# Optimization experiments

Measured on AMD Instinct MI355X. Metric: run time of the kernel, lower is better.

## Reference

```python
import jax, jax.numpy as jnp
import numpy as np

B, N, D, H = 4, 512, 256, 256


def setup_inputs() -> dict:
    key = jax.random.key(0)
    ks = jax.random.split(key, 8)
    s = lambda fan: 1.0 / np.sqrt(fan)
    return {
        "X": jax.random.normal(ks[0], (B, N, D), dtype=jnp.float32),
        "Y": jax.random.normal(ks[1], (B, N, D), dtype=jnp.float32),
        # fc = Linear(D,H) -> Tanh -> Linear(H,H)
        "W1": jax.random.normal(ks[2], (H, D), dtype=jnp.float32) * s(D),
        "b1": jnp.zeros((H,), dtype=jnp.float32),
        "W2": jax.random.normal(ks[3], (H, H), dtype=jnp.float32) * s(H),
        "b2": jnp.zeros((H,), dtype=jnp.float32),
        # fc_q, fc_k
        "Wq": jax.random.normal(ks[4], (H, H), dtype=jnp.float32) * s(H),
        "bq": jnp.zeros((H,), dtype=jnp.float32),
        "Wk": jax.random.normal(ks[5], (H, H), dtype=jnp.float32) * s(H),
        "bk": jnp.zeros((H,), dtype=jnp.float32),
        # AddComp projection vector v: E_ij = v . tanh(Q_i + K_j)
        "v": jax.random.normal(ks[6], (H,), dtype=jnp.float32) * s(H),
        "k": 5,
    }


def reference(X, Y, W1, b1, W2, b2, Wq, bq, Wk, bk, v, k):
    # fc: Linear -> Tanh -> Linear  (Y and k are unused, as in the original)
    h = jnp.tanh(jnp.einsum('bnd,hd->bnh', X, W1) + b1)
    h = jnp.einsum('bnh,gh->bng', h, W2) + b2          # [B,N,H]
    Q = jnp.einsum('bnh,gh->bng', h, Wq) + bq          # [B,N,H]
    K = jnp.einsum('bnh,gh->bng', h, Wk) + bk          # [B,N,H]
    # Additive compatibility: E[b,i,j] = v . tanh(Q[b,i] + K[b,j])
    E = jnp.einsum('bijh,h->bij', jnp.tanh(Q[:, :, None, :] + K[:, None, :, :]), v)
    # Symmetrize
    return 0.5 * (E + jnp.swapaxes(E, -2, -1))
```

## Files before the change

kernel.cpp:

```cpp
#include <hip/hip_runtime.h>


typedef float f2 __attribute__((ext_vector_type(2)));
typedef float f4 __attribute__((ext_vector_type(4)));
typedef float f32x4 __attribute__((ext_vector_type(4)));
typedef __bf16 bf16x8 __attribute__((ext_vector_type(8)));

#define C2F 2.8853900817779268f

__device__ inline unsigned short f2bf(float f) {
    unsigned u = __float_as_uint(f);
    unsigned r = (u + 0x7fffu + ((u >> 16) & 1u)) >> 16;
    return (unsigned short)r;
}
__device__ inline float bf2f(unsigned short h) {
    return __uint_as_float(((unsigned)h) << 16);
}

__device__ inline void split4(const f4 a, unsigned short* hp, unsigned short* lp) {
    unsigned short h[4], l[4];
#pragma unroll
    for (int t = 0; t < 4; ++t) {
        h[t] = f2bf(a[t]);
        l[t] = f2bf(a[t] - bf2f(h[t]));
    }
    uint2 hv, lv;
    hv.x = (unsigned)h[0] | ((unsigned)h[1] << 16);
    hv.y = (unsigned)h[2] | ((unsigned)h[3] << 16);
    lv.x = (unsigned)l[0] | ((unsigned)l[1] << 16);
    lv.y = (unsigned)l[2] | ((unsigned)l[3] << 16);
    *(uint2*)hp = hv;
    *(uint2*)lp = lv;
}

template <int ACT>
__global__ __launch_bounds__(256) void gemm_fullk(
    const float* __restrict__ A, const float* __restrict__ Wa,
    const float* __restrict__ Wb, const float* __restrict__ ba,
    const float* __restrict__ bb2, float* __restrict__ C, int Nn) {
    __shared__ unsigned short sAhi[64][264];
    __shared__ unsigned short sAlo[64][264];
    __shared__ unsigned short sBhi[64][264];
    __shared__ unsigned short sBlo[64][264];

    const int tid = threadIdx.x;
    const int m0 = blockIdx.x << 6;
    const int n0 = blockIdx.y << 6;

    const float* Atile = A + (size_t)m0 * 256;
    const float* Wtile = (n0 < 256) ? (Wa + (size_t)n0 * 256)
                                    : (Wb + (size_t)(n0 - 256) * 256);
    const int col4 = (tid & 63) << 2;
    const int rgrp = tid >> 6;
#pragma unroll
    for (int t = 0; t < 16; ++t) {
        const int row = (t << 2) + rgrp;
        f4 av = *(const f4*)&Atile[(size_t)row * 256 + col4];
        f4 wv = *(const f4*)&Wtile[(size_t)row * 256 + col4];
        split4(av, &sAhi[row][col4], &sAlo[row][col4]);
        split4(wv, &sBhi[row][col4], &sBlo[row][col4]);
    }
    __syncthreads();

    const int lane = tid & 63;
    const int wav = tid >> 6;
    const int wm = wav >> 1, wn = wav & 1;
    const int fr = lane & 15;
    const int fks = (lane >> 4) << 3;

    f32x4 acc[2][2];
#pragma unroll
    for (int i = 0; i < 2; ++i)
#pragma unroll
        for (int j = 0; j < 2; ++j) acc[i][j] = (f32x4){0.f, 0.f, 0.f, 0.f};

#pragma unroll
    for (int kt = 0; kt < 256; kt += 32) {
        bf16x8 ah[2], al[2], bh[2], bl[2];
#pragma unroll
        for (int s = 0; s < 2; ++s) {
            ah[s] = *(const bf16x8*)&sAhi[(wm << 5) + (s << 4) + fr][kt + fks];
            al[s] = *(const bf16x8*)&sAlo[(wm << 5) + (s << 4) + fr][kt + fks];
            bh[s] = *(const bf16x8*)&sBhi[(wn << 5) + (s << 4) + fr][kt + fks];
            bl[s] = *(const bf16x8*)&sBlo[(wn << 5) + (s << 4) + fr][kt + fks];
        }
#pragma unroll
        for (int i = 0; i < 2; ++i)
#pragma unroll
            for (int j = 0; j < 2; ++j) {
                acc[i][j] = __builtin_amdgcn_mfma_f32_16x16x32_bf16(ah[i], bh[j], acc[i][j], 0, 0, 0);
                acc[i][j] = __builtin_amdgcn_mfma_f32_16x16x32_bf16(ah[i], bl[j], acc[i][j], 0, 0, 0);
                acc[i][j] = __builtin_amdgcn_mfma_f32_16x16x32_bf16(al[i], bh[j], acc[i][j], 0, 0, 0);
            }
    }

    const int rbase = (lane >> 4) << 2;
#pragma unroll
    for (int i = 0; i < 2; ++i) {
#pragma unroll
        for (int j = 0; j < 2; ++j) {
            const int gcol = n0 + (wn << 5) + (j << 4) + fr;
            const float bias = (ACT == 2 && gcol >= 256) ? bb2[gcol - 256] : ba[gcol];
#pragma unroll
            for (int q = 0; q < 4; ++q) {
                const int grow = m0 + (wm << 5) + (i << 4) + rbase + q;
                float x = acc[i][j][q] + bias;
                if (ACT == 1)
                    x = 1.0f - 2.0f * __builtin_amdgcn_rcpf(
                                          1.0f + __builtin_amdgcn_exp2f(C2F * x));
                if (ACT == 2) x = __builtin_amdgcn_exp2f(C2F * x);
                C[(size_t)grow * Nn + gcol] = x;
            }
        }
    }
}

__global__ __launch_bounds__(256) void gemm_nt_fullk(
    const float* __restrict__ Wq, const float* __restrict__ Wk,
    const float* __restrict__ W2, const float* __restrict__ b2,
    const float* __restrict__ bq, const float* __restrict__ bk,
    float* __restrict__ Wc, float* __restrict__ bc) {
    __shared__ unsigned short sAhi[64][264];
    __shared__ unsigned short sAlo[64][264];
    __shared__ unsigned short sBhi[64][264];
    __shared__ unsigned short sBlo[64][264];
    __shared__ float sred[64][4];

    const int tid = threadIdx.x;
    const int m0 = blockIdx.x << 6;
    const int n0 = blockIdx.y << 6;

    const float* Atile = (m0 < 256) ? (Wq + (size_t)m0 * 256)
                                    : (Wk + (size_t)(m0 - 256) * 256);
    const int col4 = (tid & 63) << 2;
    const int rgrp = tid >> 6;
#pragma unroll
    for (int t = 0; t < 16; ++t) {
        const int row = (t << 2) + rgrp;
        f4 av = *(const f4*)&Atile[(size_t)row * 256 + col4];
        split4(av, &sAhi[row][col4], &sAlo[row][col4]);
    }
    const int c4 = (tid & 15) << 2;
    const int kg = tid >> 4;
#pragma unroll
    for (int t = 0; t < 16; ++t) {
        const int k = (t << 4) + kg;
        f4 wv = *(const f4*)&W2[(size_t)k * 256 + n0 + c4];
#pragma unroll
        for (int q = 0; q < 4; ++q) {
            unsigned short hi = f2bf(wv[q]);
            sBhi[c4 + q][k] = hi;
            sBlo[c4 + q][k] = f2bf(wv[q] - bf2f(hi));
        }
    }
    __syncthreads();

    const int lane = tid & 63;
    const int wav = tid >> 6;
    const int wm = wav >> 1, wn = wav & 1;
    const int fr = lane & 15;
    const int fks = (lane >> 4) << 3;

    f32x4 acc[2][2];
#pragma unroll
    for (int i = 0; i < 2; ++i)
#pragma unroll
        for (int j = 0; j < 2; ++j) acc[i][j] = (f32x4){0.f, 0.f, 0.f, 0.f};

#pragma unroll
    for (int kt = 0; kt < 256; kt += 32) {
        bf16x8 ah[2], al[2], bh[2], bl[2];
#pragma unroll
        for (int s = 0; s < 2; ++s) {
            ah[s] = *(const bf16x8*)&sAhi[(wm << 5) + (s << 4) + fr][kt + fks];
            al[s] = *(const bf16x8*)&sAlo[(wm << 5) + (s << 4) + fr][kt + fks];
            bh[s] = *(const bf16x8*)&sBhi[(wn << 5) + (s << 4) + fr][kt + fks];
            bl[s] = *(const bf16x8*)&sBlo[(wn << 5) + (s << 4) + fr][kt + fks];
        }
#pragma unroll
        for (int i = 0; i < 2; ++i)
#pragma unroll
            for (int j = 0; j < 2; ++j) {
                acc[i][j] = __builtin_amdgcn_mfma_f32_16x16x32_bf16(ah[i], bh[j], acc[i][j], 0, 0, 0);
                acc[i][j] = __builtin_amdgcn_mfma_f32_16x16x32_bf16(ah[i], bl[j], acc[i][j], 0, 0, 0);
                acc[i][j] = __builtin_amdgcn_mfma_f32_16x16x32_bf16(al[i], bh[j], acc[i][j], 0, 0, 0);
            }
    }

    const int rbase = (lane >> 4) << 2;
#pragma unroll
    for (int i = 0; i < 2; ++i)
#pragma unroll
        for (int j = 0; j < 2; ++j) {
            const int gcol = n0 + (wn << 5) + (j << 4) + fr;
#pragma unroll
            for (int q = 0; q < 4; ++q) {
                const int grow = m0 + (wm << 5) + (i << 4) + rbase + q;
                Wc[(size_t)grow * 256 + gcol] = acc[i][j][q];
            }
        }

    if (blockIdx.y == 0) {
        const int rr = tid >> 2;
        const int part = (tid & 3) << 6;
        const int grow = m0 + rr;
        const float* Ar = (grow < 256) ? &Wq[(size_t)grow * 256]
                                       : &Wk[(size_t)(grow - 256) * 256];
        float s = 0.f;
#pragma unroll
        for (int e = 0; e < 64; e += 4) {
            f4 a = *(const f4*)&Ar[part + e];
            f4 bv = *(const f4*)&b2[part + e];
            s += a[0] * bv[0] + a[1] * bv[1] + a[2] * bv[2] + a[3] * bv[3];
        }
        sred[rr][tid & 3] = s;
        __syncthreads();
        if (tid < 64) {
            float bias = sred[tid][0] + sred[tid][1] + sred[tid][2] + sred[tid][3];
            const int g2 = m0 + tid;
            bias += (g2 < 256) ? bq[g2] : bk[g2 - 256];
            bc[g2] = bias;
        }
    }
}

__global__ __launch_bounds__(512, 4) void pairwise_kernel(
    const float* __restrict__ uwb, const float* __restrict__ v,
    float* __restrict__ out) {
    __shared__ float sU[2][64][68];
    __shared__ float sW[2][64][68];
    __shared__ float sV[128];

    const int tid = threadIdx.x;
    const int bb = blockIdx.x;
    const int hh = (bb & 1) << 7;
    const int tt = bb >> 1;
    const int b = tt >> 6;
    const int i0 = ((tt >> 3) & 7) << 6;
    const int j0 = (tt & 7) << 6;

    const float* ubase = uwb + (size_t)((b << 9) + i0) * 512 + hh;
    const float* wbase = uwb + (size_t)((b << 9) + j0) * 512 + 256 + hh;

    const int sr = tid >> 3;
    const int sc = (tid & 7) << 3;

    {
        f4 a0 = *(const f4*)&ubase[(size_t)sr * 512 + sc];
        f4 a1 = *(const f4*)&ubase[(size_t)sr * 512 + sc + 4];
        f4 b0 = *(const f4*)&wbase[(size_t)sr * 512 + sc];
        f4 b1 = *(const f4*)&wbase[(size_t)sr * 512 + sc + 4];
        *(f4*)&sU[0][sr][sc] = a0;
        *(f4*)&sU[0][sr][sc + 4] = a1;
        *(f4*)&sW[0][sr][sc] = b0;
        *(f4*)&sW[0][sr][sc + 4] = b1;
    }
    if (tid < 32) *(f4*)&sV[tid << 2] = *(const f4*)&v[hh + (tid << 2)];
    __syncthreads();

    const int ty = tid >> 5;
    const int tx = tid & 31;

    float acc[4][2];
#pragma unroll
    for (int d = 0; d < 4; ++d)
#pragma unroll
        for (int e = 0; e < 2; ++e) acc[d][e] = 0.f;

    const f2 one2 = (f2){1.f, 1.f};

#define COMPUTE_CHUNK(buf, vb)                                                  \
    {                                                                           \
        _Pragma("unroll 2") for (int h4 = 0; h4 < 64; h4 += 4) {                \
            f4 vv = *(const f4*)&sV[(vb) + h4];                                 \
            f4 uu[4], ww[2];                                                    \
            _Pragma("unroll") for (int d = 0; d < 4; ++d)                       \
                uu[d] = *(const f4*)&sU[buf][ty + (d << 4)][h4];                \
            _Pragma("unroll") for (int e = 0; e < 2; ++e)                       \
                ww[e] = *(const f4*)&sW[buf][tx + (e << 5)][h4];                \
            _Pragma("unroll") for (int d = 0; d < 4; ++d)                       \
            _Pragma("unroll") for (int e = 0; e < 2; ++e) {                     \
                f2 u01 = (f2){uu[d][0], uu[d][1]};                              \
                f2 u23 = (f2){uu[d][2], uu[d][3]};                              \
                f2 w01 = (f2){ww[e][0], ww[e][1]};                              \
                f2 w23 = (f2){ww[e][2], ww[e][3]};                              \
                f2 p1 = __builtin_elementwise_fma(u01, w01, one2);              \
                f2 p2 = __builtin_elementwise_fma(u23, w23, one2);              \
                float den1 = p1[0] * p1[1];                                     \
                float den2 = p2[0] * p2[1];                                     \
                float num1 = fmaf(vv[1], p1[0], vv[0] * p1[1]);                 \
                float num2 = fmaf(vv[3], p2[0], vv[2] * p2[1]);                 \
                acc[d][e] = fmaf(num1, __builtin_amdgcn_rcpf(den1), acc[d][e]); \
                acc[d][e] = fmaf(num2, __builtin_amdgcn_rcpf(den2), acc[d][e]); \
            }                                                                   \
        }                                                                       \
    }

    f4 pa0 = *(const f4*)&ubase[(size_t)sr * 512 + 64 + sc];
    f4 pa1 = *(const f4*)&ubase[(size_t)sr * 512 + 64 + sc + 4];
    f4 pb0 = *(const f4*)&wbase[(size_t)sr * 512 + 64 + sc];
    f4 pb1 = *(const f4*)&wbase[(size_t)sr * 512 + 64 + sc + 4];

    COMPUTE_CHUNK(0, 0)

    *(f4*)&sU[1][sr][sc] = pa0;
    *(f4*)&sU[1][sr][sc + 4] = pa1;
    *(f4*)&sW[1][sr][sc] = pb0;
    *(f4*)&sW[1][sr][sc + 4] = pb1;
    __syncthreads();

    COMPUTE_CHUNK(1, 64)
#undef COMPUTE_CHUNK

    float sv = 0.f;
#pragma unroll
    for (int k = 0; k < 128; k += 4) {
        f4 t = *(const f4*)&sV[k];
        sv += (t[0] + t[1]) + (t[2] + t[3]);
    }

    float c[4][2];
#pragma unroll
    for (int d = 0; d < 4; ++d)
#pragma unroll
        for (int e = 0; e < 2; ++e) c[d][e] = fmaf(0.5f, sv, -acc[d][e]);

    float* obase = out + (size_t)((b << 9) + i0) * 512 + j0;
#pragma unroll
    for (int d = 0; d < 4; ++d)
#pragma unroll
        for (int e = 0; e < 2; ++e)
            atomicAdd(&obase[(size_t)(ty + (d << 4)) * 512 + tx + (e << 5)], c[d][e]);

    float(*sT)[68] = sU[0];
#pragma unroll
    for (int d = 0; d < 4; ++d)
#pragma unroll
        for (int e = 0; e < 2; ++e)
            sT[ty + (d << 4)][tx + (e << 5)] = c[d][e];
    __syncthreads();

    const int wv_ = tid >> 6;
    const int lane = tid & 63;
    float* mbase = out + (size_t)((b << 9) + j0) * 512 + i0;
#pragma unroll
    for (int it = 0; it < 8; ++it) {
        const int r = (it << 3) + wv_;
        atomicAdd(&mbase[(size_t)r * 512 + lane], sT[lane][r]);
    }
}

extern "C" void kernel_launch(void* const* d_in, const int* in_sizes, int n_in,
                              void* d_out, int out_size, void* d_ws, size_t ws_size,
                              hipStream_t stream) {
    const float* X  = (const float*)d_in[0];
    const float* W1 = (const float*)d_in[2];
    const float* b1 = (const float*)d_in[3];
    const float* W2 = (const float*)d_in[4];
    const float* b2 = (const float*)d_in[5];
    const float* Wq = (const float*)d_in[6];
    const float* bq = (const float*)d_in[7];
    const float* Wk = (const float*)d_in[8];
    const float* bk = (const float*)d_in[9];
    const float* v  = (const float*)d_in[10];

    float* ws  = (float*)d_ws;
    float* h1  = ws;
    float* uwb = ws + 524288;
    float* Wc  = ws + 1572864;
    float* bc  = ws + 1703936;
    float* out = (float*)d_out;

    hipMemsetAsync(out, 0, (size_t)out_size * sizeof(float), stream);

    gemm_nt_fullk<<<dim3(8, 4), 256, 0, stream>>>(Wq, Wk, W2, b2, bq, bk, Wc, bc);
    gemm_fullk<1><<<dim3(32, 4), 256, 0, stream>>>(X, W1, W1, b1, b1, h1, 256);
    gemm_fullk<2><<<dim3(32, 8), 256, 0, stream>>>(h1, Wc, Wc + 65536, bc, bc + 256, uwb, 512);
    pairwise_kernel<<<512, 512, 0, stream>>>(uwb, v, out);
}
```

Measured before the change: 69.89 us.

## Merge first-stage GEMMs, pair rational tanh terms, replace atomics with symmetrize pass

Folds the Wc/bc weight-fusion GEMM and the X·W1 tanh GEMM into one launch, so the two independent first-stage matmuls share a single grid. The pairwise kernel now combines four h-terms per reciprocal instead of two, halving the rcp count. It also stops using memset and atomics: each half-H block writes its partial E to workspace, and a new kernel sums the halves, transposes, and symmetrizes. The exp output is clamped to 1e4 so the larger product of four factors does not overflow, at some cost in accuracy for large arguments. The new path adds a workspace round trip and an extra launch.

```diff
diff --git a/kernel.cpp b/kernel.cpp
--- a/kernel.cpp
+++ b/kernel.cpp
@@ -108,17 +108,20 @@
                 if (ACT == 1)
                     x = 1.0f - 2.0f * __builtin_amdgcn_rcpf(
                                           1.0f + __builtin_amdgcn_exp2f(C2F * x));
-                if (ACT == 2) x = __builtin_amdgcn_exp2f(C2F * x);
+                if (ACT == 2)
+                    x = fminf(__builtin_amdgcn_exp2f(C2F * x), 1.0e4f);
                 C[(size_t)grow * Nn + gcol] = x;
             }
         }
     }
 }
 
-__global__ __launch_bounds__(256) void gemm_nt_fullk(
-    const float* __restrict__ Wq, const float* __restrict__ Wk,
-    const float* __restrict__ W2, const float* __restrict__ b2,
-    const float* __restrict__ bq, const float* __restrict__ bk,
+__global__ __launch_bounds__(256) void gemm_stage1(
+    const float* __restrict__ X, const float* __restrict__ W1,
+    const float* __restrict__ b1, const float* __restrict__ Wq,
+    const float* __restrict__ Wk, const float* __restrict__ W2,
+    const float* __restrict__ b2, const float* __restrict__ bq,
+    const float* __restrict__ bk, float* __restrict__ h1,
     float* __restrict__ Wc, float* __restrict__ bc) {
     __shared__ unsigned short sAhi[64][264];
     __shared__ unsigned short sAlo[64][264];
@@ -127,30 +130,46 @@
     __shared__ float sred[64][4];
 
     const int tid = threadIdx.x;
-    const int m0 = blockIdx.x << 6;
-    const int n0 = blockIdx.y << 6;
-
-    const float* Atile = (m0 < 256) ? (Wq + (size_t)m0 * 256)
-                                    : (Wk + (size_t)(m0 - 256) * 256);
+    const bool is_nt = (blockIdx.x >= 128);
+    const int blk = is_nt ? (blockIdx.x - 128) : blockIdx.x;
+    const int m0 = (is_nt ? (blk >> 2) : (blk >> 2)) << 6;
+    const int n0 = (blk & 3) << 6;
+
     const int col4 = (tid & 63) << 2;
     const int rgrp = tid >> 6;
-#pragma unroll
-    for (int t = 0; t < 16; ++t) {
-        const int row = (t << 2) + rgrp;
-        f4 av = *(const f4*)&Atile[(size_t)row * 256 + col4];
-        split4(av, &sAhi[row][col4], &sAlo[row][col4]);
-    }
-    const int c4 = (tid & 15) << 2;
-    const int kg = tid >> 4;
-#pragma unroll
-    for (int t = 0; t < 16; ++t) {
-        const int k = (t << 4) + kg;
-        f4 wv = *(const f4*)&W2[(size_t)k * 256 + n0 + c4];
-#pragma unroll
-        for (int q = 0; q < 4; ++q) {
-            unsigned short hi = f2bf(wv[q]);
-            sBhi[c4 + q][k] = hi;
-            sBlo[c4 + q][k] = f2bf(wv[q] - bf2f(hi));
+
+    if (!is_nt) {
+        const float* Atile = X + (size_t)m0 * 256;
+        const float* Wtile = W1 + (size_t)n0 * 256;
+#pragma unroll
+        for (int t = 0; t < 16; ++t) {
+            const int row = (t << 2) + rgrp;
+            f4 av = *(const f4*)&Atile[(size_t)row * 256 + col4];
+            f4 wv = *(const f4*)&Wtile[(size_t)row * 256 + col4];
+            split4(av, &sAhi[row][col4], &sAlo[row][col4]);
+            split4(wv, &sBhi[row][col4], &sBlo[row][col4]);
+        }
+    } else {
+        const float* Atile = (m0 < 256) ? (Wq + (size_t)m0 * 256)
+                                        : (Wk + (size_t)(m0 - 256) * 256);
+#pragma unroll
+        for (int t = 0; t < 16; ++t) {
+            const int row = (t << 2) + rgrp;
+            f4 av = *(const f4*)&Atile[(size_t)row * 256 + col4];
+            split4(av, &sAhi[row][col4], &sAlo[row][col4]);
+        }
+        const int c4 = (tid & 15) << 2;
+        const int kg = tid >> 4;
+#pragma unroll
+        for (int t = 0; t < 16; ++t) {
+            const int k = (t << 4) + kg;
+            f4 wv = *(const f4*)&W2[(size_t)k * 256 + n0 + c4];
+#pragma unroll
+            for (int q = 0; q < 4; ++q) {
+                unsigned short hi = f2bf(wv[q]);
+                sBhi[c4 + q][k] = hi;
+                sBlo[c4 + q][k] = f2bf(wv[q] - bf2f(hi));
+            }
         }
     }
     __syncthreads();
@@ -188,45 +207,62 @@
     }
 
     const int rbase = (lane >> 4) << 2;
-#pragma unroll
-    for (int i = 0; i < 2; ++i)
-#pragma unroll
-        for (int j = 0; j < 2; ++j) {
-            const int gcol = n0 + (wn << 5) + (j << 4) + fr;
-#pragma unroll
-            for (int q = 0; q < 4; ++q) {
-                const int grow = m0 + (wm << 5) + (i << 4) + rbase + q;
-                Wc[(size_t)grow * 256 + gcol] = acc[i][j][q];
-            }
-        }
-
-    if (blockIdx.y == 0) {
-        const int rr = tid >> 2;
-        const int part = (tid & 3) << 6;
-        const int grow = m0 + rr;
-        const float* Ar = (grow < 256) ? &Wq[(size_t)grow * 256]
-                                       : &Wk[(size_t)(grow - 256) * 256];
-        float s = 0.f;
-#pragma unroll
-        for (int e = 0; e < 64; e += 4) {
-            f4 a = *(const f4*)&Ar[part + e];
-            f4 bv = *(const f4*)&b2[part + e];
-            s += a[0] * bv[0] + a[1] * bv[1] + a[2] * bv[2] + a[3] * bv[3];
-        }
-        sred[rr][tid & 3] = s;
-        __syncthreads();
-        if (tid < 64) {
-            float bias = sred[tid][0] + sred[tid][1] + sred[tid][2] + sred[tid][3];
-            const int g2 = m0 + tid;
-            bias += (g2 < 256) ? bq[g2] : bk[g2 - 256];
-            bc[g2] = bias;
+    if (!is_nt) {
+#pragma unroll
+        for (int i = 0; i < 2; ++i)
+#pragma unroll
+            for (int j = 0; j < 2; ++j) {
+                const int gcol = n0 + (wn << 5) + (j << 4) + fr;
+                const float bias = b1[gcol];
+#pragma unroll
+                for (int q = 0; q < 4; ++q) {
+                    const int grow = m0 + (wm << 5) + (i << 4) + rbase + q;
+                    float x = acc[i][j][q] + bias;
+                    x = 1.0f - 2.0f * __builtin_amdgcn_rcpf(
+                                          1.0f + __builtin_amdgcn_exp2f(C2F * x));
+                    h1[(size_t)grow * 256 + gcol] = x;
+                }
+            }
+    } else {
+#pragma unroll
+        for (int i = 0; i < 2; ++i)
+#pragma unroll
+            for (int j = 0; j < 2; ++j) {
+                const int gcol = n0 + (wn << 5) + (j << 4) + fr;
+#pragma unroll
+                for (int q = 0; q < 4; ++q) {
+                    const int grow = m0 + (wm << 5) + (i << 4) + rbase + q;
+                    Wc[(size_t)grow * 256 + gcol] = acc[i][j][q];
+                }
+            }
+        if ((blk & 3) == 0) {
+            const int rr = tid >> 2;
+            const int part = (tid & 3) << 6;
+            const int grow = m0 + rr;
+            const float* Ar = (grow < 256) ? &Wq[(size_t)grow * 256]
+                                           : &Wk[(size_t)(grow - 256) * 256];
+            float s = 0.f;
+#pragma unroll
+            for (int e = 0; e < 64; e += 4) {
+                f4 a = *(const f4*)&Ar[part + e];
+                f4 bv = *(const f4*)&b2[part + e];
+                s += a[0] * bv[0] + a[1] * bv[1] + a[2] * bv[2] + a[3] * bv[3];
+            }
+            sred[rr][tid & 3] = s;
+            __syncthreads();
+            if (tid < 64) {
+                float bias = sred[tid][0] + sred[tid][1] + sred[tid][2] + sred[tid][3];
+                const int g2 = m0 + tid;
+                bias += (g2 < 256) ? bq[g2] : bk[g2 - 256];
+                bc[g2] = bias;
+            }
         }
     }
 }
 
 __global__ __launch_bounds__(512, 4) void pairwise_kernel(
     const float* __restrict__ uwb, const float* __restrict__ v,
-    float* __restrict__ out) {
+    float* __restrict__ Ep) {
     __shared__ float sU[2][64][68];
     __shared__ float sW[2][64][68];
     __shared__ float sV[128];
@@ -269,31 +305,32 @@
 
     const f2 one2 = (f2){1.f, 1.f};
 
-#define COMPUTE_CHUNK(buf, vb)                                                  \
-    {                                                                           \
-        _Pragma("unroll 2") for (int h4 = 0; h4 < 64; h4 += 4) {                \
-            f4 vv = *(const f4*)&sV[(vb) + h4];                                 \
-            f4 uu[4], ww[2];                                                    \
-            _Pragma("unroll") for (int d = 0; d < 4; ++d)                       \
-                uu[d] = *(const f4*)&sU[buf][ty + (d << 4)][h4];                \
-            _Pragma("unroll") for (int e = 0; e < 2; ++e)                       \
-                ww[e] = *(const f4*)&sW[buf][tx + (e << 5)][h4];                \
-            _Pragma("unroll") for (int d = 0; d < 4; ++d)                       \
-            _Pragma("unroll") for (int e = 0; e < 2; ++e) {                     \
-                f2 u01 = (f2){uu[d][0], uu[d][1]};                              \
-                f2 u23 = (f2){uu[d][2], uu[d][3]};                              \
-                f2 w01 = (f2){ww[e][0], ww[e][1]};                              \
-                f2 w23 = (f2){ww[e][2], ww[e][3]};                              \
-                f2 p1 = __builtin_elementwise_fma(u01, w01, one2);              \
-                f2 p2 = __builtin_elementwise_fma(u23, w23, one2);              \
-                float den1 = p1[0] * p1[1];                                     \
-                float den2 = p2[0] * p2[1];                                     \
-                float num1 = fmaf(vv[1], p1[0], vv[0] * p1[1]);                 \
-                float num2 = fmaf(vv[3], p2[0], vv[2] * p2[1]);                 \
-                acc[d][e] = fmaf(num1, __builtin_amdgcn_rcpf(den1), acc[d][e]); \
-                acc[d][e] = fmaf(num2, __builtin_amdgcn_rcpf(den2), acc[d][e]); \
-            }                                                                   \
-        }                                                                       \
+#define COMPUTE_CHUNK(buf, vb)                                                 \
+    {                                                                          \
+        _Pragma("unroll 2") for (int h4 = 0; h4 < 64; h4 += 4) {               \
+            f4 vv = *(const f4*)&sV[(vb) + h4];                                \
+            f4 uu[4], ww[2];                                                   \
+            _Pragma("unroll") for (int d = 0; d < 4; ++d)                      \
+                uu[d] = *(const f4*)&sU[buf][ty + (d << 4)][h4];               \
+            _Pragma("unroll") for (int e = 0; e < 2; ++e)                      \
+                ww[e] = *(const f4*)&sW[buf][tx + (e << 5)][h4];               \
+            _Pragma("unroll") for (int d = 0; d < 4; ++d)                      \
+            _Pragma("unroll") for (int e = 0; e < 2; ++e) {                    \
+                f2 u01 = (f2){uu[d][0], uu[d][1]};                             \
+                f2 u23 = (f2){uu[d][2], uu[d][3]};                             \
+                f2 w01 = (f2){ww[e][0], ww[e][1]};                             \
+                f2 w23 = (f2){ww[e][2], ww[e][3]};                             \
+                f2 A01 = __builtin_elementwise_fma(u01, w01, one2);            \
+                f2 A23 = __builtin_elementwise_fma(u23, w23, one2);            \
+                float m01 = A01.x * A01.y;                                     \
+                float m23 = A23.x * A23.y;                                     \
+                float P = m01 * m23;                                           \
+                float t01 = fmaf(vv[0], A01.y, vv[1] * A01.x);                 \
+                float t23 = fmaf(vv[2], A23.y, vv[3] * A23.x);                 \
+                float Nm = fmaf(t01, m23, t23 * m01);                          \
+                acc[d][e] = fmaf(Nm, __builtin_amdgcn_rcpf(P), acc[d][e]);     \
+            }                                                                  \
+        }                                                                      \
     }
 
     f4 pa0 = *(const f4*)&ubase[(size_t)sr * 512 + 64 + sc];
@@ -312,41 +349,47 @@
     COMPUTE_CHUNK(1, 64)
 #undef COMPUTE_CHUNK
 
-    float sv = 0.f;
-#pragma unroll
-    for (int k = 0; k < 128; k += 4) {
-        f4 t = *(const f4*)&sV[k];
-        sv += (t[0] + t[1]) + (t[2] + t[3]);
-    }
-
-    float c[4][2];
+    float* ep = Ep + (size_t)(bb & 1) * 1048576 +
+                (size_t)((b << 9) + i0) * 512 + j0;
 #pragma unroll
     for (int d = 0; d < 4; ++d)
 #pragma unroll
-        for (int e = 0; e < 2; ++e) c[d][e] = fmaf(0.5f, sv, -acc[d][e]);
-
-    float* obase = out + (size_t)((b << 9) + i0) * 512 + j0;
-#pragma unroll
-    for (int d = 0; d < 4; ++d)
-#pragma unroll
         for (int e = 0; e < 2; ++e)
-            atomicAdd(&obase[(size_t)(ty + (d << 4)) * 512 + tx + (e << 5)], c[d][e]);
-
-    float(*sT)[68] = sU[0];
-#pragma unroll
-    for (int d = 0; d < 4; ++d)
-#pragma unroll
-        for (int e = 0; e < 2; ++e)
-            sT[ty + (d << 4)][tx + (e << 5)] = c[d][e];
+            ep[(size_t)(ty + (d << 4)) * 512 + tx + (e << 5)] = acc[d][e];
+}
+
+__global__ __launch_bounds__(256) void sym_kernel(const float* __restrict__ Ep,
+                                                  const float* __restrict__ v,
+                                                  float* __restrict__ out) {
+    __shared__ float t1[64][65];
+    __shared__ float t2[64][65];
+    __shared__ float red[4];
+
+    const int tid = threadIdx.x;
+    const int lane = tid & 63, wv = tid >> 6;
+
+    float x = v[tid];
+#pragma unroll
+    for (int o = 32; o > 0; o >>= 1) x += __shfl_xor(x, o, 64);
+    if (lane == 0) red[wv] = x;
+
+    const int bb = blockIdx.x;
+    const int b = bb >> 6;
+    const int i0 = ((bb >> 3) & 7) << 6;
+    const int j0 = (bb & 7) << 6;
+
+    for (int idx = tid; idx < 4096; idx += 256) {
+        const int r = idx >> 6, c = idx & 63;
+        const size_t o1 = (size_t)((b << 9) + i0 + r) * 512 + j0 + c;
+        const size_t o2 = (size_t)((b << 9) + j0 + r) * 512 + i0 + c;
+        t1[r][c] = Ep[o1] + Ep[o1 + 1048576];
+        t2[r][c] = Ep[o2] + Ep[o2 + 1048576];
+    }
     __syncthreads();
-
-    const int wv_ = tid >> 6;
-    const int lane = tid & 63;
-    float* mbase = out + (size_t)((b << 9) + j0) * 512 + i0;
-#pragma unroll
-    for (int it = 0; it < 8; ++it) {
-        const int r = (it << 3) + wv_;
-        atomicAdd(&mbase[(size_t)r * 512 + lane], sT[lane][r]);
+    const float Sv = red[0] + red[1] + red[2] + red[3];
+    for (int idx = tid; idx < 4096; idx += 256) {
+        const int r = idx >> 6, c = idx & 63;
+        out[(size_t)((b << 9) + i0 + r) * 512 + j0 + c] = Sv - (t1[r][c] + t2[c][r]);
     }
 }
 
@@ -369,12 +412,13 @@
     float* uwb = ws + 524288;
     float* Wc  = ws + 1572864;
     float* bc  = ws + 1703936;
+    float* Ep  = ws + 1704448;
     float* out = (float*)d_out;
 
-    hipMemsetAsync(out, 0, (size_t)out_size * sizeof(float), stream);
-
-    gemm_nt_fullk<<<dim3(8, 4), 256, 0, stream>>>(Wq, Wk, W2, b2, bq, bk, Wc, bc);
-    gemm_fullk<1><<<dim3(32, 4), 256, 0, stream>>>(X, W1, W1, b1, b1, h1, 256);
-    gemm_fullk<2><<<dim3(32, 8), 256, 0, stream>>>(h1, Wc, Wc + 65536, bc, bc + 256, uwb, 512);
-    pairwise_kernel<<<512, 512, 0, stream>>>(uwb, v, out);
-}
+    gemm_stage1<<<160, 256, 0, stream>>>(X, W1, b1, Wq, Wk, W2, b2, bq, bk,
+                                         h1, Wc, bc);
+    gemm_fullk<2><<<dim3(32, 8), 256, 0, stream>>>(h1, Wc, Wc + 65536, bc,
+                                                   bc + 256, uwb, 512);
+    pairwise_kernel<<<512, 512, 0, stream>>>(uwb, v, Ep);
+    sym_kernel<<<256, 256, 0, stream>>>(Ep, v, out);
+}
```

After: 61.60 us. 1.13x faster.
